# Optimization experiments

Measured on AMD Instinct MI355X. Metric: run time of the kernel, lower is better.

## Reference

```python
import jax, jax.numpy as jnp
import numpy as np

SEQ_LEN = 2048
NUM_GLOBAL = 32
NEG_INF = float('-inf')


def _build_mask(seq_len=SEQ_LEN, num_global=NUM_GLOBAL):
    # Causal mask: triu(ones).T == lower-triangular ones; zeros -> -inf, ones -> 0.
    m = np.where(np.tril(np.ones((seq_len, seq_len), dtype=np.float32)) == 1.0, 0.0, NEG_INF)
    # Deterministic 'random.sample' of global tokens (fixed for reproducibility).
    rng = np.random.default_rng(0)
    gtok = rng.choice(seq_len, size=num_global, replace=False)
    m[:, gtok] = 0.0
    m[gtok, :] = 0.0
    return jnp.asarray(m)


def setup_inputs() -> dict:
    key = jax.random.key(0)
    ks = jax.random.split(key, 9)
    B, S, D_IN, D_QK = 8, SEQ_LEN, 1024, 128
    return {
        'q': jax.random.normal(ks[0], (B, S, D_IN), dtype=jnp.float32),
        'k': jax.random.normal(ks[1], (B, S, D_IN), dtype=jnp.float32),
        'v': jax.random.normal(ks[2], (B, S, D_IN), dtype=jnp.float32),
        'Wq': jax.random.normal(ks[3], (D_QK, D_IN), dtype=jnp.float32) * 0.02,
        'bq': jax.random.normal(ks[4], (D_QK,), dtype=jnp.float32) * 0.02,
        'Wk': jax.random.normal(ks[5], (D_QK, D_IN), dtype=jnp.float32) * 0.02,
        'bk': jax.random.normal(ks[6], (D_QK,), dtype=jnp.float32) * 0.02,
        'Wv': jax.random.normal(ks[7], (D_QK, D_IN), dtype=jnp.float32) * 0.02,
        'bv': jax.random.normal(ks[8], (D_QK,), dtype=jnp.float32) * 0.02,
    }


def reference(q, k, v, Wq, bq, Wk, bk, Wv, bv):
    # Linear projections (torch nn.Linear: x @ W.T + b)
    Q = jnp.einsum('bsd,qd->bsq', q, Wq) + bq   # [B,S,dq]
    K = jnp.einsum('bsd,qd->bsq', k, Wk) + bk   # [B,S,dk]
    V = jnp.einsum('bsd,qd->bsq', v, Wv) + bv   # [B,S,dk]
    mask = _build_mask()                        # [S,S] static causal+global
    scale = K.shape[-1] ** 0.5
    scores = jnp.einsum('bqd,bkd->bqk', Q, K)   # dense QK^T [B,S,S]
    scores = (scores + mask) / scale            # (-inf stays -inf)
    attn = jax.nn.softmax(scores, axis=-1)
    return jnp.einsum('bqk,bkd->bqd', attn, V)
```

## Files before the change

kernel.cpp:

```cpp
#include <hip/hip_runtime.h>
#include <cstdint>

constexpr int SEQ  = 2048;
constexpr int DIN  = 1024;
constexpr int DQK  = 128;
constexpr int NB   = 8;
constexpr int MTOT = NB * SEQ;
constexpr float INV_SCALE = 0.08838834764831845f;

typedef __attribute__((ext_vector_type(8))) short  short8;
typedef __attribute__((ext_vector_type(4))) float  floatx4;
typedef __attribute__((ext_vector_type(4))) int    intx4;

struct GM { unsigned long long w[32]; };

static void compute_gtok(unsigned long long bits[32]) {
  typedef unsigned __int128 u128;
  uint32_t pool[4];
  uint32_t hc = 0x43b0d7e5u;
  auto hashmix = [&hc](uint32_t v) -> uint32_t {
    v ^= hc; hc *= 0x931e8875u; v *= hc; v ^= v >> 16; return v;
  };
  auto mixf = [](uint32_t x, uint32_t y) -> uint32_t {
    uint32_t r = x * 0xca01f9ddu - y * 0x4973f715u;
    r ^= r >> 16; return r;
  };
  pool[0] = hashmix(0u);
  for (int i = 1; i < 4; ++i) pool[i] = hashmix(0u);
  for (int s = 0; s < 4; ++s)
    for (int d = 0; d < 4; ++d)
      if (s != d) pool[d] = mixf(pool[d], hashmix(pool[s]));
  uint32_t hb = 0x8b51f9ddu;
  uint32_t st[8];
  for (int i = 0; i < 8; ++i) {
    uint32_t dv = pool[i & 3];
    dv ^= hb; hb *= 0x58f38dedu; dv *= hb; dv ^= dv >> 16;
    st[i] = dv;
  }
  uint64_t sv[4];
  for (int i = 0; i < 4; ++i)
    sv[i] = (uint64_t)st[2 * i] | ((uint64_t)st[2 * i + 1] << 32);
  const u128 MUL = ((u128)2549297995355413924ULL << 64) | (u128)4865540595714422341ULL;
  u128 initstate = ((u128)sv[0] << 64) | sv[1];
  u128 initseq   = ((u128)sv[2] << 64) | sv[3];
  u128 state = 0;
  u128 inc = (initseq << 1) | 1;
  state = state * MUL + inc;
  state += initstate;
  state = state * MUL + inc;
  bool has32 = false; uint32_t cache32 = 0;
  auto next64 = [&]() -> uint64_t {
    state = state * MUL + inc;
    uint64_t hi = (uint64_t)(state >> 64);
    uint64_t lo = (uint64_t)state;
    unsigned rot = (unsigned)(state >> 122);
    uint64_t x = hi ^ lo;
    return (x >> rot) | (x << ((64u - rot) & 63u));
  };
  auto next32 = [&]() -> uint32_t {
    if (has32) { has32 = false; return cache32; }
    uint64_t n = next64();
    has32 = true; cache32 = (uint32_t)(n >> 32);
    return (uint32_t)n;
  };
  bool in_set[SEQ];
  for (int i = 0; i < SEQ; ++i) in_set[i] = false;
  for (uint32_t j = 2016; j < 2048; ++j) {
    uint32_t rng_excl = j + 1;
    uint64_t m = (uint64_t)next32() * rng_excl;
    uint32_t leftover = (uint32_t)m;
    if (leftover < rng_excl) {
      uint32_t threshold = (0xFFFFFFFFu - j) % rng_excl;
      while (leftover < threshold) {
        m = (uint64_t)next32() * rng_excl;
        leftover = (uint32_t)m;
      }
    }
    uint32_t val = (uint32_t)(m >> 32);
    if (in_set[val]) in_set[j] = true;
    else in_set[val] = true;
  }
  for (int i = 0; i < 32; ++i) bits[i] = 0ULL;
  for (int t = 0; t < SEQ; ++t)
    if (in_set[t]) bits[t >> 6] |= (1ULL << (t & 63));
}

__device__ __forceinline__ unsigned short bfr(float x) {
  unsigned u = __float_as_uint(x);
  return (unsigned short)((u + 0x7FFFu + ((u >> 16) & 1u)) >> 16);
}
__device__ __forceinline__ float bf2f(unsigned short h) {
  return __uint_as_float(((unsigned)h) << 16);
}
__device__ __forceinline__ void ldsld16(const void* g, void* l) {
  __builtin_amdgcn_global_load_lds(
      (const __attribute__((address_space(1))) unsigned int*)g,
      (__attribute__((address_space(3))) unsigned int*)l, 16, 0, 0);
}
__device__ __forceinline__ bool gbit(const GM& g, int j) {
  return (g.w[j >> 6] >> (j & 63)) & 1ULL;
}
__device__ __forceinline__ unsigned long long pk4(const unsigned short h[4]) {
  return (unsigned long long)h[0] | ((unsigned long long)h[1] << 16) |
         ((unsigned long long)h[2] << 32) | ((unsigned long long)h[3] << 48);
}

__global__ __launch_bounds__(256) void wconv_kernel(
    const float* __restrict__ Wq, const float* __restrict__ Wk, const float* __restrict__ Wv,
    unsigned short* __restrict__ Whi, unsigned short* __restrict__ Wlo) {
  const float* W = blockIdx.y == 0 ? Wq : blockIdx.y == 1 ? Wk : Wv;
  size_t base = (size_t)blockIdx.y * DQK * DIN;
  int e = (blockIdx.x * 256 + threadIdx.x) * 4;
  float4 x = *(const float4*)&W[e];
  float xs[4] = {x.x, x.y, x.z, x.w};
  unsigned short h[4], l[4];
#pragma unroll
  for (int i = 0; i < 4; ++i) { h[i] = bfr(xs[i]); l[i] = bfr(xs[i] - bf2f(h[i])); }
  *(unsigned long long*)&Whi[base + e] = pk4(h);
  *(unsigned long long*)&Wlo[base + e] = pk4(l);
}

__global__ __launch_bounds__(256, 2) void proj_kernel(
    const float* __restrict__ xq, const float* __restrict__ xk, const float* __restrict__ xv,
    const unsigned short* __restrict__ Whi, const unsigned short* __restrict__ Wlo,
    const float* __restrict__ bq, const float* __restrict__ bk, const float* __restrict__ bv,
    unsigned short* __restrict__ Qb, unsigned short* __restrict__ Kb,
    unsigned short* __restrict__ Vth, unsigned short* __restrict__ Vtl) {
  const int which = blockIdx.y;
  const float* X    = which == 0 ? xq : which == 1 ? xk : xv;
  const float* bias = which == 0 ? bq : which == 1 ? bk : bv;
  const int m0 = blockIdx.x * 128;

  __shared__ unsigned short sm[4][8192];

  const int tid = threadIdx.x;
  const int w = tid >> 6, lane = tid & 63, l15 = lane & 15, quad = lane >> 4;
  const int mh = (w >> 1) * 64, nh = (w & 1) * 64;

  floatx4 acc[4][4] = {};
  float biasv[4];
#pragma unroll
  for (int j = 0; j < 4; ++j) biasv[j] = bias[nh + j * 16 + l15];

  const unsigned short* WhiP = Whi + (size_t)which * DQK * DIN;
  const unsigned short* WloP = Wlo + (size_t)which * DQK * DIN;

  for (int kb = 0; kb < DIN; kb += 64) {
    __syncthreads();
#pragma unroll
    for (int i = 0; i < 8; ++i) {
      int f = tid + i * 256;
      int r = f >> 4, c4 = f & 15;
      float4 x = *(const float4*)&X[(size_t)(m0 + r) * DIN + kb + c4 * 4];
      float xs[4] = {x.x, x.y, x.z, x.w};
      unsigned short hh[4], ll[4];
#pragma unroll
      for (int t = 0; t < 4; ++t) { hh[t] = bfr(xs[t]); ll[t] = bfr(xs[t] - bf2f(hh[t])); }
      int off = r * 64 + (((c4 >> 1) ^ (r & 7)) * 8) + (c4 & 1) * 4;
      *(unsigned long long*)&sm[0][off] = pk4(hh);
      *(unsigned long long*)&sm[1][off] = pk4(ll);
    }
#pragma unroll
    for (int i = 0; i < 8; ++i) {
      int c = w * 8 + i;
      int plane = c >> 4, cc = c & 15;
      int F = cc * 1024 + lane * 16;
      int n = F >> 7, gs = (F >> 4) & 7, gl = gs ^ (n & 7);
      const unsigned short* gp = (plane ? WloP : WhiP) + (size_t)n * DIN + kb + gl * 8;
      ldsld16(gp, (char*)&sm[2 + plane][0] + cc * 1024);
    }
    __syncthreads();
#pragma unroll
    for (int ks = 0; ks < 2; ++ks) {
      short8 Ah[4], Al[4], Bh[4], Bl[4];
#pragma unroll
      for (int ms = 0; ms < 4; ++ms) {
        int off = (mh + ms * 16 + l15) * 64 + (((ks * 4 + quad) ^ (l15 & 7)) * 8);
        Ah[ms] = *(const short8*)&sm[0][off];
        Al[ms] = *(const short8*)&sm[1][off];
      }
#pragma unroll
      for (int ns = 0; ns < 4; ++ns) {
        int off = (nh + ns * 16 + l15) * 64 + (((ks * 4 + quad) ^ (l15 & 7)) * 8);
        Bh[ns] = *(const short8*)&sm[2][off];
        Bl[ns] = *(const short8*)&sm[3][off];
      }
#pragma unroll
      for (int i = 0; i < 4; ++i)
#pragma unroll
        for (int j = 0; j < 4; ++j) {
          floatx4 c = acc[i][j];
          c = __builtin_amdgcn_mfma_f32_16x16x32_bf16(Ah[i], Bh[j], c, 0, 0, 0);
          c = __builtin_amdgcn_mfma_f32_16x16x32_bf16(Ah[i], Bl[j], c, 0, 0, 0);
          c = __builtin_amdgcn_mfma_f32_16x16x32_bf16(Al[i], Bh[j], c, 0, 0, 0);
          acc[i][j] = c;
        }
    }
  }

  if (which < 2) {
    unsigned short* O = which == 0 ? Qb : Kb;
#pragma unroll
    for (int i = 0; i < 4; ++i)
#pragma unroll
      for (int j = 0; j < 4; ++j)
#pragma unroll
        for (int r = 0; r < 4; ++r) {
          int m = mh + i * 16 + quad * 4 + r;
          int n = nh + j * 16 + l15;
          O[(size_t)(m0 + m) * DQK + n] = bfr(acc[i][j][r] + biasv[j]);
        }
  } else {
    __syncthreads();
    unsigned short* VH = &sm[0][0];
    unsigned short* VL = &sm[2][0];
#pragma unroll
    for (int i = 0; i < 4; ++i)
#pragma unroll
      for (int j = 0; j < 4; ++j)
#pragma unroll
        for (int r = 0; r < 4; ++r) {
          int s = mh + i * 16 + quad * 4 + r;
          int d = nh + j * 16 + l15;
          float v = acc[i][j][r] + biasv[j];
          unsigned short h = bfr(v);
          unsigned short lo = bfr(v - bf2f(h));
          int off = d * 128 + (((s >> 3) ^ (d & 15)) * 8) + (s & 7);
          VH[off] = h; VL[off] = lo;
        }
    __syncthreads();
    int b = m0 >> 11, s0 = m0 & 2047;
#pragma unroll
    for (int i = 0; i < 8; ++i) {
      int cch = i * 256 + tid;
      int d = cch >> 4, gI = cch & 15;
      int loff = d * 128 + ((gI ^ (d & 15)) * 8);
      intx4 vh = *(const intx4*)&VH[loff];
      intx4 vl = *(const intx4*)&VL[loff];
      size_t go = ((size_t)b * DQK + d) * SEQ + s0 + gI * 8;
      *(intx4*)&Vth[go] = vh;
      *(intx4*)&Vtl[go] = vl;
    }
  }
}

__global__ __launch_bounds__(256, 2) void attn_kernel(
    const unsigned short* __restrict__ Qb, const unsigned short* __restrict__ Kb,
    const unsigned short* __restrict__ Vth, const unsigned short* __restrict__ Vtl,
    float* __restrict__ Out, GM g, unsigned int t64) {
  __shared__ unsigned short Ks[64 * 128];
  __shared__ unsigned short Vh[128 * 64];
  __shared__ unsigned short Vl[128 * 64];
  __shared__ unsigned short Ph[4][16 * 80];
  __shared__ unsigned short Pl[4][16 * 80];

  const int tid = threadIdx.x;
  const int w = tid >> 6, lane = tid & 63, l15 = lane & 15, quad = lane >> 4;
  const int b = blockIdx.y, qt = blockIdx.x, qs = qt * 64;

  short8 qf[4];
  const unsigned short* Qrow = Qb + ((size_t)(b * SEQ + qs + w * 16 + l15)) * DQK;
#pragma unroll
  for (int j = 0; j < 4; ++j) qf[j] = *(const short8*)&Qrow[j * 32 + quad * 8];

  int rowi[4]; bool growb[4];
#pragma unroll
  for (int r = 0; r < 4; ++r) {
    rowi[r] = qs + w * 16 + quad * 4 + r;
    growb[r] = gbit(g, rowi[r]);
  }

  floatx4 o[8] = {};
  float m_r[4] = {-1e30f, -1e30f, -1e30f, -1e30f};
  float l_r[4] = {0.f, 0.f, 0.f, 0.f};

  const bool qhasg = (t64 >> qt) & 1;
  const unsigned short* KbB = Kb  + (size_t)b * SEQ * DQK;
  const unsigned short* VhB = Vth + (size_t)b * DQK * SEQ;
  const unsigned short* VlB = Vtl + (size_t)b * DQK * SEQ;

  for (int kt = 0; kt < 32; ++kt) {
    const int ks0 = kt * 64;
    if (!((ks0 <= qs + 63) || ((t64 >> kt) & 1) || qhasg)) continue;

    __syncthreads();
#pragma unroll
    for (int i = 0; i < 12; ++i) {
      int c = w * 12 + i;
      if (c < 16) {
        int F = c * 1024 + lane * 16;
        int r = F >> 8, gs = (F >> 4) & 15, gl = gs ^ (r & 15);
        ldsld16(KbB + (size_t)(ks0 + r) * DQK + gl * 8, (char*)Ks + c * 1024);
      } else if (c < 32) {
        int cc = c - 16;
        int F = cc * 1024 + lane * 16;
        int d = F >> 7, gs = (F >> 4) & 7, gl = gs ^ (d & 7);
        ldsld16(VhB + (size_t)d * SEQ + ks0 + gl * 8, (char*)Vh + cc * 1024);
      } else {
        int cc = c - 32;
        int F = cc * 1024 + lane * 16;
        int d = F >> 7, gs = (F >> 4) & 7, gl = gs ^ (d & 7);
        ldsld16(VlB + (size_t)d * SEQ + ks0 + gl * 8, (char*)Vl + cc * 1024);
      }
    }
    __syncthreads();

    floatx4 S[4];
#pragma unroll
    for (int c4 = 0; c4 < 4; ++c4) {
      floatx4 s = {0.f, 0.f, 0.f, 0.f};
#pragma unroll
      for (int j = 0; j < 4; ++j) {
        short8 kf = *(const short8*)&Ks[(c4 * 16 + l15) * 128 + (((j * 4 + quad) ^ l15) * 8)];
        s = __builtin_amdgcn_mfma_f32_16x16x32_bf16(qf[j], kf, s, 0, 0, 0);
      }
      S[c4] = s;
    }

    float z[4][4];
    float mx[4] = {-1e30f, -1e30f, -1e30f, -1e30f};
#pragma unroll
    for (int c4 = 0; c4 < 4; ++c4) {
      int col = ks0 + c4 * 16 + l15;
      bool cg = gbit(g, col);
#pragma unroll
      for (int r = 0; r < 4; ++r) {
        bool ok = (col <= rowi[r]) || cg || growb[r];
        float zz = ok ? S[c4][r] * INV_SCALE : -1e30f;
        z[c4][r] = zz;
        mx[r] = fmaxf(mx[r], zz);
      }
    }
#pragma unroll
    for (int d = 1; d < 16; d <<= 1)
#pragma unroll
      for (int r = 0; r < 4; ++r) mx[r] = fmaxf(mx[r], __shfl_xor(mx[r], d));
    float alpha[4], rs[4] = {0.f, 0.f, 0.f, 0.f};
#pragma unroll
    for (int r = 0; r < 4; ++r) {
      float mn = fmaxf(m_r[r], mx[r]);
      alpha[r] = __expf(m_r[r] - mn);
      m_r[r] = mn;
    }
    float p[4][4];
#pragma unroll
    for (int c4 = 0; c4 < 4; ++c4)
#pragma unroll
      for (int r = 0; r < 4; ++r) {
        float pp = __expf(z[c4][r] - m_r[r]);
        p[c4][r] = pp;
        rs[r] += pp;
      }
#pragma unroll
    for (int d = 1; d < 16; d <<= 1)
#pragma unroll
      for (int r = 0; r < 4; ++r) rs[r] += __shfl_xor(rs[r], d);
#pragma unroll
    for (int r = 0; r < 4; ++r) l_r[r] = l_r[r] * alpha[r] + rs[r];
#pragma unroll
    for (int n = 0; n < 8; ++n)
#pragma unroll
      for (int r = 0; r < 4; ++r) o[n][r] *= alpha[r];

#pragma unroll
    for (int c4 = 0; c4 < 4; ++c4)
#pragma unroll
      for (int r = 0; r < 4; ++r) {
        unsigned short h = bfr(p[c4][r]);
        unsigned short lo = bfr(p[c4][r] - bf2f(h));
        int off = (quad * 4 + r) * 80 + c4 * 16 + l15;
        Ph[w][off] = h; Pl[w][off] = lo;
      }
    short8 pf[2], pg[2];
#pragma unroll
    for (int kq = 0; kq < 2; ++kq) {
      int off = l15 * 80 + kq * 32 + quad * 8;
      pf[kq] = *(const short8*)&Ph[w][off];
      pg[kq] = *(const short8*)&Pl[w][off];
    }

#pragma unroll
    for (int n = 0; n < 8; ++n) {
      int drow = n * 16 + l15;
#pragma unroll
      for (int kq = 0; kq < 2; ++kq) {
        int off = drow * 64 + (((kq * 4 + quad) ^ (drow & 7)) * 8);
        short8 vhf = *(const short8*)&Vh[off];
        short8 vlf = *(const short8*)&Vl[off];
        floatx4 c = o[n];
        c = __builtin_amdgcn_mfma_f32_16x16x32_bf16(pf[kq], vhf, c, 0, 0, 0);
        c = __builtin_amdgcn_mfma_f32_16x16x32_bf16(pg[kq], vhf, c, 0, 0, 0);
        c = __builtin_amdgcn_mfma_f32_16x16x32_bf16(pf[kq], vlf, c, 0, 0, 0);
        o[n] = c;
      }
    }
  }

  float invl[4];
#pragma unroll
  for (int r = 0; r < 4; ++r) invl[r] = 1.0f / l_r[r];
  float* Ob = Out + (size_t)b * SEQ * DQK;
#pragma unroll
  for (int n = 0; n < 8; ++n)
#pragma unroll
    for (int r = 0; r < 4; ++r)
      Ob[(size_t)(qs + w * 16 + quad * 4 + r) * DQK + n * 16 + l15] = o[n][r] * invl[r];
}

extern "C" void kernel_launch(void* const* d_in, const int* in_sizes, int n_in,
                              void* d_out, int out_size, void* d_ws, size_t ws_size,
                              hipStream_t stream) {
  const float* q  = (const float*)d_in[0];
  const float* k  = (const float*)d_in[1];
  const float* v  = (const float*)d_in[2];
  const float* Wq = (const float*)d_in[3];
  const float* bq = (const float*)d_in[4];
  const float* Wk = (const float*)d_in[5];
  const float* bk = (const float*)d_in[6];
  const float* Wv = (const float*)d_in[7];
  const float* bv = (const float*)d_in[8];
  float* out = (float*)d_out;

  unsigned short* Qb  = (unsigned short*)d_ws;
  unsigned short* Kb2 = Qb  + (size_t)MTOT * DQK;
  unsigned short* Vth = Kb2 + (size_t)MTOT * DQK;
  unsigned short* Vtl = Vth + (size_t)MTOT * DQK;
  unsigned short* Whi = Vtl + (size_t)MTOT * DQK;
  unsigned short* Wlo = Whi + (size_t)3 * DQK * DIN;

  GM g;
  compute_gtok(g.w);
  unsigned int t64 = 0;
  for (int t = 0; t < 32; ++t) if (g.w[t] != 0ULL) t64 |= (1u << t);

  hipLaunchKernelGGL(wconv_kernel, dim3(128, 3), dim3(256), 0, stream,
                     Wq, Wk, Wv, Whi, Wlo);
  hipLaunchKernelGGL(proj_kernel, dim3(128, 3), dim3(256), 0, stream,
                     q, k, v, Whi, Wlo, bq, bk, bv, Qb, Kb2, Vth, Vtl);
  hipLaunchKernelGGL(attn_kernel, dim3(32, 8), dim3(256), 0, stream,
                     Qb, Kb2, Vth, Vtl, out, g, t64);
}
```

Measured before the change: 323.4 us.

## Split attention KV loop across two blocks and merge partials; truncate bf16 splits

Attention work is split so each query tile runs in two blocks, each handling alternating key tiles. Each block writes unnormalized partial outputs plus row max and sum, and a new merge kernel combines them with a log-sum-exp rescale. This raises the grid from 256 to 512 blocks to fill more CUs and balance the causal load. Separately, the hi/lo bf16 split now truncates with perm instructions instead of round-to-nearest, cutting ALU work in projection and softmax. The cost is an extra launch plus partial-output traffic, and the split precision changes slightly.

```diff
diff --git a/kernel.cpp b/kernel.cpp
--- a/kernel.cpp
+++ b/kernel.cpp
@@ -85,10 +85,6 @@
     if (in_set[t]) bits[t >> 6] |= (1ULL << (t & 63));
 }
 
-__device__ __forceinline__ unsigned short bfr(float x) {
-  unsigned u = __float_as_uint(x);
-  return (unsigned short)((u + 0x7FFFu + ((u >> 16) & 1u)) >> 16);
-}
 __device__ __forceinline__ float bf2f(unsigned short h) {
   return __uint_as_float(((unsigned)h) << 16);
 }
@@ -100,9 +96,23 @@
 __device__ __forceinline__ bool gbit(const GM& g, int j) {
   return (g.w[j >> 6] >> (j & 63)) & 1ULL;
 }
-__device__ __forceinline__ unsigned long long pk4(const unsigned short h[4]) {
-  return (unsigned long long)h[0] | ((unsigned long long)h[1] << 16) |
-         ((unsigned long long)h[2] << 32) | ((unsigned long long)h[3] << 48);
+__device__ __forceinline__ void split4(float4 x, unsigned hw[2], unsigned lw[2]) {
+  unsigned u0 = __float_as_uint(x.x), u1 = __float_as_uint(x.y);
+  unsigned u2 = __float_as_uint(x.z), u3 = __float_as_uint(x.w);
+  hw[0] = __builtin_amdgcn_perm(u1, u0, 0x07060302u);
+  hw[1] = __builtin_amdgcn_perm(u3, u2, 0x07060302u);
+  unsigned r0 = __float_as_uint(x.x - __uint_as_float(u0 & 0xFFFF0000u));
+  unsigned r1 = __float_as_uint(x.y - __uint_as_float(u1 & 0xFFFF0000u));
+  unsigned r2 = __float_as_uint(x.z - __uint_as_float(u2 & 0xFFFF0000u));
+  unsigned r3 = __float_as_uint(x.w - __uint_as_float(u3 & 0xFFFF0000u));
+  lw[0] = __builtin_amdgcn_perm(r1, r0, 0x07060302u);
+  lw[1] = __builtin_amdgcn_perm(r3, r2, 0x07060302u);
+}
+__device__ __forceinline__ void split1(float v, unsigned short& h, unsigned short& l) {
+  unsigned u = __float_as_uint(v);
+  h = (unsigned short)(u >> 16);
+  float rr = v - __uint_as_float(u & 0xFFFF0000u);
+  l = (unsigned short)(__float_as_uint(rr) >> 16);
 }
 
 __global__ __launch_bounds__(256) void wconv_kernel(
@@ -112,12 +122,10 @@
   size_t base = (size_t)blockIdx.y * DQK * DIN;
   int e = (blockIdx.x * 256 + threadIdx.x) * 4;
   float4 x = *(const float4*)&W[e];
-  float xs[4] = {x.x, x.y, x.z, x.w};
-  unsigned short h[4], l[4];
-#pragma unroll
-  for (int i = 0; i < 4; ++i) { h[i] = bfr(xs[i]); l[i] = bfr(xs[i] - bf2f(h[i])); }
-  *(unsigned long long*)&Whi[base + e] = pk4(h);
-  *(unsigned long long*)&Wlo[base + e] = pk4(l);
+  unsigned hw[2], lw[2];
+  split4(x, hw, lw);
+  *(uint2*)&Whi[base + e] = make_uint2(hw[0], hw[1]);
+  *(uint2*)&Wlo[base + e] = make_uint2(lw[0], lw[1]);
 }
 
 __global__ __launch_bounds__(256, 2) void proj_kernel(
@@ -152,13 +160,11 @@
       int f = tid + i * 256;
       int r = f >> 4, c4 = f & 15;
       float4 x = *(const float4*)&X[(size_t)(m0 + r) * DIN + kb + c4 * 4];
-      float xs[4] = {x.x, x.y, x.z, x.w};
-      unsigned short hh[4], ll[4];
-#pragma unroll
-      for (int t = 0; t < 4; ++t) { hh[t] = bfr(xs[t]); ll[t] = bfr(xs[t] - bf2f(hh[t])); }
+      unsigned hw[2], lw[2];
+      split4(x, hw, lw);
       int off = r * 64 + (((c4 >> 1) ^ (r & 7)) * 8) + (c4 & 1) * 4;
-      *(unsigned long long*)&sm[0][off] = pk4(hh);
-      *(unsigned long long*)&sm[1][off] = pk4(ll);
+      *(uint2*)&sm[0][off] = make_uint2(hw[0], hw[1]);
+      *(uint2*)&sm[1][off] = make_uint2(lw[0], lw[1]);
     }
 #pragma unroll
     for (int i = 0; i < 8; ++i) {
@@ -208,7 +214,10 @@
         for (int r = 0; r < 4; ++r) {
           int m = mh + i * 16 + quad * 4 + r;
           int n = nh + j * 16 + l15;
-          O[(size_t)(m0 + m) * DQK + n] = bfr(acc[i][j][r] + biasv[j]);
+          float v = acc[i][j][r] + biasv[j];
+          O[(size_t)(m0 + m) * DQK + n] =
+              (unsigned short)((__float_as_uint(v) + 0x7FFFu +
+                                ((__float_as_uint(v) >> 16) & 1u)) >> 16);
         }
   } else {
     __syncthreads();
@@ -223,8 +232,8 @@
           int s = mh + i * 16 + quad * 4 + r;
           int d = nh + j * 16 + l15;
           float v = acc[i][j][r] + biasv[j];
-          unsigned short h = bfr(v);
-          unsigned short lo = bfr(v - bf2f(h));
+          unsigned short h, lo;
+          split1(v, h, lo);
           int off = d * 128 + (((s >> 3) ^ (d & 15)) * 8) + (s & 7);
           VH[off] = h; VL[off] = lo;
         }
@@ -247,7 +256,7 @@
 __global__ __launch_bounds__(256, 2) void attn_kernel(
     const unsigned short* __restrict__ Qb, const unsigned short* __restrict__ Kb,
     const unsigned short* __restrict__ Vth, const unsigned short* __restrict__ Vtl,
-    float* __restrict__ Out, GM g, unsigned int t64) {
+    float* __restrict__ Opart, float2* __restrict__ ML, GM g, unsigned int t64) {
   __shared__ unsigned short Ks[64 * 128];
   __shared__ unsigned short Vh[128 * 64];
   __shared__ unsigned short Vl[128 * 64];
@@ -256,7 +265,9 @@
 
   const int tid = threadIdx.x;
   const int w = tid >> 6, lane = tid & 63, l15 = lane & 15, quad = lane >> 4;
-  const int b = blockIdx.y, qt = blockIdx.x, qs = qt * 64;
+  const int b = blockIdx.y;
+  const int qt = blockIdx.x >> 1, half = blockIdx.x & 1;
+  const int qs = qt * 64;
 
   short8 qf[4];
   const unsigned short* Qrow = Qb + ((size_t)(b * SEQ + qs + w * 16 + l15)) * DQK;
@@ -279,7 +290,7 @@
   const unsigned short* VhB = Vth + (size_t)b * DQK * SEQ;
   const unsigned short* VlB = Vtl + (size_t)b * DQK * SEQ;
 
-  for (int kt = 0; kt < 32; ++kt) {
+  for (int kt = half; kt < 32; kt += 2) {
     const int ks0 = kt * 64;
     if (!((ks0 <= qs + 63) || ((t64 >> kt) & 1) || qhasg)) continue;
 
@@ -366,8 +377,8 @@
     for (int c4 = 0; c4 < 4; ++c4)
 #pragma unroll
       for (int r = 0; r < 4; ++r) {
-        unsigned short h = bfr(p[c4][r]);
-        unsigned short lo = bfr(p[c4][r] - bf2f(h));
+        unsigned short h, lo;
+        split1(p[c4][r], h, lo);
         int off = (quad * 4 + r) * 80 + c4 * 16 + l15;
         Ph[w][off] = h; Pl[w][off] = lo;
       }
@@ -396,15 +407,36 @@
     }
   }
 
-  float invl[4];
-#pragma unroll
-  for (int r = 0; r < 4; ++r) invl[r] = 1.0f / l_r[r];
-  float* Ob = Out + (size_t)b * SEQ * DQK;
+  const size_t grp = (size_t)(b * 32 + qt) * 2 + half;
+  float* Op = Opart + grp * 64 * 128;
 #pragma unroll
   for (int n = 0; n < 8; ++n)
 #pragma unroll
     for (int r = 0; r < 4; ++r)
-      Ob[(size_t)(qs + w * 16 + quad * 4 + r) * DQK + n * 16 + l15] = o[n][r] * invl[r];
+      Op[(w * 16 + quad * 4 + r) * 128 + n * 16 + l15] = o[n][r];
+  if (l15 == 0) {
+#pragma unroll
+    for (int r = 0; r < 4; ++r)
+      ML[grp * 64 + w * 16 + quad * 4 + r] = make_float2(m_r[r], l_r[r]);
+  }
+}
+
+__global__ __launch_bounds__(256) void merge_kernel(
+    const float* __restrict__ Opart, const float2* __restrict__ ML,
+    float* __restrict__ Out) {
+  const int t = threadIdx.x;
+  const int row = blockIdx.x * 2 + (t >> 7);
+  const int col = t & 127;
+  const int grp = row >> 6;
+  const int rin = row & 63;
+  const size_t i0 = ((size_t)grp * 2 + 0) * 64 + rin;
+  const size_t i1 = ((size_t)grp * 2 + 1) * 64 + rin;
+  const float2 ml0 = ML[i0], ml1 = ML[i1];
+  const float m = fmaxf(ml0.x, ml1.x);
+  const float w0 = __expf(ml0.x - m), w1 = __expf(ml1.x - m);
+  const float denom = w0 * ml0.y + w1 * ml1.y;
+  const float o0 = Opart[i0 * 128 + col], o1 = Opart[i1 * 128 + col];
+  Out[(size_t)row * 128 + col] = (w0 * o0 + w1 * o1) / denom;
 }
 
 extern "C" void kernel_launch(void* const* d_in, const int* in_sizes, int n_in,
@@ -427,6 +459,8 @@
   unsigned short* Vtl = Vth + (size_t)MTOT * DQK;
   unsigned short* Whi = Vtl + (size_t)MTOT * DQK;
   unsigned short* Wlo = Whi + (size_t)3 * DQK * DIN;
+  float*  Opart = (float*)(Wlo + (size_t)3 * DQK * DIN);
+  float2* ML    = (float2*)(Opart + (size_t)2 * MTOT * DQK);
 
   GM g;
   compute_gtok(g.w);
@@ -437,6 +471,8 @@
                      Wq, Wk, Wv, Whi, Wlo);
   hipLaunchKernelGGL(proj_kernel, dim3(128, 3), dim3(256), 0, stream,
                      q, k, v, Whi, Wlo, bq, bk, bv, Qb, Kb2, Vth, Vtl);
-  hipLaunchKernelGGL(attn_kernel, dim3(32, 8), dim3(256), 0, stream,
-                     Qb, Kb2, Vth, Vtl, out, g, t64);
-}
+  hipLaunchKernelGGL(attn_kernel, dim3(64, 8), dim3(256), 0, stream,
+                     Qb, Kb2, Vth, Vtl, Opart, ML, g, t64);
+  hipLaunchKernelGGL(merge_kernel, dim3(MTOT / 2), dim3(256), 0, stream,
+                     Opart, ML, out);
+}
```

Result: faster. 293.5 us (-9.2%).
